# Kernel tuning notes

Hardware: AMD Instinct MI355X
Metric: run time of the kernel (lower is better)

The kernel has to match this reference:

```python
import jax, jax.numpy as jnp
import numpy as np

N, IN_DIM, H1, H2 = 12288, 512, 256, 128

def setup_inputs() -> dict:
    key = jax.random.key(0)
    k = jax.random.split(key, 6)
    glorot = lambda kk, fi, fo: jax.random.normal(kk, (fi, fo), jnp.float32) * np.sqrt(2.0 / (fi + fo))
    return {
        "X": jax.random.normal(k[0], (N, IN_DIM), jnp.float32),
        "adj": jax.random.uniform(k[1], (N, N), jnp.float32) / N,  # scaled like a normalized adjacency
        "noise": jax.random.normal(k[2], (N, H2), jnp.float32),
        "W0": glorot(k[3], IN_DIM, H1),
        "W_mu": glorot(k[4], H1, H2),
        "W_logstd": glorot(k[5], H1, H2),
    }

def reference(X, adj, noise, W0, W_mu, W_logstd):
    # GraphConvSparse layer 1: relu(adj @ (X @ W0))
    hidden = jax.nn.relu(adj @ (X @ W0))            # [N, H1]
    # mean / logstd heads (identity activation)
    mean = adj @ (hidden @ W_mu)                    # [N, H2]
    logstd = adj @ (hidden @ W_logstd)              # [N, H2]
    # reparameterization
    Z = noise * jnp.exp(logstd) + mean              # [N, H2]
    # dot-product decode
    A_pred = jax.nn.sigmoid(Z @ Z.T)                # [N, N]
    return A_pred
```

## Files before the change

kernel.cpp:

```cpp
#include <hip/hip_runtime.h>
#include <hip/hip_fp8.h>
#include <stdint.h>

#define NN 12288
#define IND 512
#define H1D 256
#define H2D 128

using bf16x8 = __attribute__((ext_vector_type(8))) short;
using f32x4  = __attribute__((ext_vector_type(4))) float;
using u32x4  = __attribute__((ext_vector_type(4))) unsigned int;

__device__ __forceinline__ unsigned short f2bf(float f){
  unsigned int u = __float_as_uint(f);
  return (unsigned short)((u + 0x7fffu + ((u >> 16) & 1u)) >> 16);
}
__device__ __forceinline__ float bf2f(unsigned short h){
  return __uint_as_float(((unsigned int)h) << 16);
}
__device__ __forceinline__ void gload_lds16(const void* g, void* l){
  __builtin_amdgcn_global_load_lds(
      (const __attribute__((address_space(1))) unsigned int*)(uintptr_t)g,
      (__attribute__((address_space(3))) unsigned int*)(unsigned int)(uintptr_t)l,
      16, 0, 0);
}
template<bool HI>
__device__ __forceinline__ unsigned cvt2(float a, float b, unsigned old){
#if __has_builtin(__builtin_amdgcn_cvt_pk_fp8_f32)
  return (unsigned)__builtin_amdgcn_cvt_pk_fp8_f32(a, b, (int)old, HI);
#else
  __hip_fp8_e4m3 pa(a), pb(b);
  unsigned v = (unsigned)pa.__x | ((unsigned)pb.__x << 8);
  return HI ? ((old & 0x0000FFFFu) | (v << 16)) : ((old & 0xFFFF0000u) | v);
#endif
}
__device__ __forceinline__ void sync0(){
  asm volatile("s_waitcnt vmcnt(0) lgkmcnt(0)" ::: "memory");
  __builtin_amdgcn_s_barrier();
  __builtin_amdgcn_sched_barrier(0);
}

__global__ __launch_bounds__(256) void k_cvt(const float* __restrict__ in,
                                             char* __restrict__ out,
                                             float scale, long n16){
  const long stride = (long)gridDim.x * 256;
  for (long i = (long)blockIdx.x * 256 + threadIdx.x; i < n16; i += stride){
    const f32x4* p = (const f32x4*)(in + i * 16);
    f32x4 a = __builtin_nontemporal_load(p);
    f32x4 b = __builtin_nontemporal_load(p + 1);
    f32x4 c = __builtin_nontemporal_load(p + 2);
    f32x4 d = __builtin_nontemporal_load(p + 3);
    u32x4 pk;
    pk[0] = cvt2<false>(a[0]*scale, a[1]*scale, 0u); pk[0] = cvt2<true>(a[2]*scale, a[3]*scale, pk[0]);
    pk[1] = cvt2<false>(b[0]*scale, b[1]*scale, 0u); pk[1] = cvt2<true>(b[2]*scale, b[3]*scale, pk[1]);
    pk[2] = cvt2<false>(c[0]*scale, c[1]*scale, 0u); pk[2] = cvt2<true>(c[2]*scale, c[3]*scale, pk[2]);
    pk[3] = cvt2<false>(d[0]*scale, d[1]*scale, 0u); pk[3] = cvt2<true>(d[2]*scale, d[3]*scale, pk[3]);
    *(u32x4*)(out + i * 16) = pk;
  }
}

__global__ __launch_bounds__(256) void k_w0t(const float* __restrict__ W0,
                                             char* __restrict__ W0T){
  __shared__ float Ls[64][65];
  const int t = (int)threadIdx.x;
  const int k0 = (int)blockIdx.x * 64;
  const int h0 = (int)blockIdx.y * 64;
  {
    const int r = t >> 2, c = (t & 3) * 16;
    const float* p = W0 + (size_t)(k0 + r) * H1D + h0 + c;
#pragma unroll
    for (int q = 0; q < 4; ++q)
      *(float4*)&Ls[r][c + q*4] = *(const float4*)(p + q*4);
  }
  __syncthreads();
  const int h = t >> 2, kc = (t & 3) * 16;
  u32x4 pk;
#pragma unroll
  for (int q = 0; q < 4; ++q){
    unsigned wv = cvt2<false>(Ls[kc+q*4+0][h], Ls[kc+q*4+1][h], 0u);
    wv = cvt2<true>(Ls[kc+q*4+2][h], Ls[kc+q*4+3][h], wv);
    pk[q] = wv;
  }
  *(u32x4*)(W0T + (size_t)(h0 + h) * IND + k0 + kc) = pk;
}

#define STAGE(BUF, SIDX) { \
  _Pragma("unroll") \
  for (int p = 0; p < 2; ++p) \
    gload_lds16(Ap + (size_t)(p*32) * lda + (size_t)(SIDX)*128, \
                Alds[BUF] + p*4096 + w*1024); \
  _Pragma("unroll") \
  for (int i = 0; i < 4; ++i) \
    gload_lds16(Bp + (size_t)(i*32) * ldb + (size_t)(SIDX)*128, \
                Blds[BUF] + i*4096 + w*1024); \
}

#define MF8(CUR) { \
  _Pragma("unroll") \
  for (int kk = 0; kk < 4; ++kk){ \
    long af[4]; long bfr[2]; \
    _Pragma("unroll") \
    for (int mi = 0; mi < 4; ++mi){ \
      int row = mi*16 + l15; \
      int off = row*128 + ((kk*32 + l16*8) ^ ((row & 7) << 4)); \
      af[mi] = *(const long*)(Alds[CUR] + off); \
    } \
    _Pragma("unroll") \
    for (int ni = 0; ni < 2; ++ni){ \
      int row = w*32 + ni*16 + l15; \
      int off = row*128 + ((kk*32 + l16*8) ^ ((row & 7) << 4)); \
      bfr[ni] = *(const long*)(Blds[CUR] + off); \
    } \
    _Pragma("unroll") \
    for (int mi = 0; mi < 4; ++mi) \
      _Pragma("unroll") \
      for (int ni = 0; ni < 2; ++ni) \
        acc[mi][ni] = __builtin_amdgcn_mfma_f32_16x16x32_fp8_fp8(af[mi], bfr[ni], acc[mi][ni], 0, 0, 0); \
  } }

template<int KSPLIT, int MODE>
__global__ __launch_bounds__(256, 3) void k_gf8(const char* __restrict__ A, int lda, int K,
                                                const char* __restrict__ Bt, int ldb,
                                                void* __restrict__ Out){
  __shared__ __align__(16) char Alds[2][64*128];
  __shared__ __align__(16) char Blds[2][128*128];
  const int t = (int)threadIdx.x;
  const int w = t >> 6, l = t & 63;
  const int l15 = l & 15, l16 = l >> 4;

  int khalf, idx;
  if (KSPLIT == 2){
    int f = (int)blockIdx.x, x = f & 7;
    khalf = x >> 2;
    idx = (f >> 3) * 4 + (x & 3);
  } else { khalf = 0; idx = (int)blockIdx.x; }
  const int m0 = (idx >> 1) * 64;
  const int nh = idx & 1;
  const size_t kb = (size_t)khalf * K;
  const int S = K >> 7;

  f32x4 acc[4][2];
#pragma unroll
  for (int mi = 0; mi < 4; ++mi)
#pragma unroll
    for (int ni = 0; ni < 2; ++ni) acc[mi][ni] = 0;

  const int swz = ((l & 7) ^ (l >> 3)) << 4;
  const char* Ap = A  + (size_t)(m0 + w*8 + (l >> 3)) * lda + kb + swz;
  const char* Bp = Bt + (size_t)(nh*128 + w*8 + (l >> 3)) * ldb + kb + swz;

  STAGE(0, 0);
  sync0();
  for (int s = 0; s < S; ++s){
    const int cur = s & 1;
    if (s + 1 < S){ if (cur == 0){ STAGE(1, s + 1); } else { STAGE(0, s + 1); } }
    if (cur == 0){ MF8(0); } else { MF8(1); }
    if (s + 1 < S) sync0();
  }

  if (MODE == 0){
    char* OutT = (char*)Out;
#pragma unroll
    for (int mi = 0; mi < 4; ++mi)
#pragma unroll
      for (int ni = 0; ni < 2; ++ni){
        int gr = m0 + mi*16 + l16*4;
        int gc = nh*128 + w*32 + ni*16 + l15;
        unsigned wd = cvt2<false>(acc[mi][ni][0], acc[mi][ni][1], 0u);
        wd = cvt2<true>(acc[mi][ni][2], acc[mi][ni][3], wd);
        *(unsigned*)(OutT + (size_t)gc * NN + gr) = wd;
      }
  } else {
    float* P = (float*)Out + (size_t)khalf * NN * H1D;
#pragma unroll
    for (int mi = 0; mi < 4; ++mi)
#pragma unroll
      for (int ni = 0; ni < 2; ++ni){
        int gr = m0 + mi*16 + l16*4;
        int gc = nh*128 + w*32 + ni*16 + l15;
#pragma unroll
        for (int v = 0; v < 4; ++v)
          P[(size_t)(gr + v) * H1D + gc] = acc[mi][ni][v];
      }
  }
}

__global__ __launch_bounds__(256) void k_combine_ht(const float* __restrict__ p0,
                                                    const float* __restrict__ p1,
                                                    char* __restrict__ HT){
  __shared__ float Ls[64][65];
  const int t = (int)threadIdx.x;
  const int n0 = (int)blockIdx.x * 64;
  const int h0 = (int)blockIdx.y * 64;
  const int lr = t >> 4, lc = (t & 15) * 4;
#pragma unroll
  for (int q = 0; q < 4; ++q){
    int n = lr + q*16;
    size_t idx = (size_t)(n0 + n) * H1D + h0 + lc;
    float4 a = *(const float4*)(p0 + idx);
    float4 b = *(const float4*)(p1 + idx);
    Ls[n][lc+0] = fmaxf(a.x + b.x, 0.f);
    Ls[n][lc+1] = fmaxf(a.y + b.y, 0.f);
    Ls[n][lc+2] = fmaxf(a.z + b.z, 0.f);
    Ls[n][lc+3] = fmaxf(a.w + b.w, 0.f);
  }
  __syncthreads();
  const int hr = t >> 2, nc = (t & 3) * 16;
  u32x4 pk;
#pragma unroll
  for (int q = 0; q < 4; ++q){
    unsigned wd = cvt2<false>(Ls[nc+q*4+0][hr], Ls[nc+q*4+1][hr], 0u);
    wd = cvt2<true>(Ls[nc+q*4+2][hr], Ls[nc+q*4+3][hr], wd);
    pk[q] = wd;
  }
  *(u32x4*)(HT + (size_t)(h0 + hr) * NN + n0 + nc) = pk;
}

__global__ __launch_bounds__(256) void k_heads(const float* __restrict__ p0,
                                               const float* __restrict__ Wmu,
                                               const float* __restrict__ Wls,
                                               const float* __restrict__ noise,
                                               unsigned short* __restrict__ Zhi,
                                               unsigned short* __restrict__ Zlo){
  __shared__ float AHs[32][256];
  __shared__ float Wms[32][128];
  __shared__ float Wlss[32][128];
  const float INV = 1.0f / 67108864.0f;
  const float* p1 = p0 + (size_t)NN * H1D;
  const int t  = (int)threadIdx.x;
  const int r0 = (int)blockIdx.x * 32;
  {
    const int r = t >> 3, c0 = (t & 7) * 32;
    size_t base = (size_t)(r0 + r) * H1D + c0;
#pragma unroll
    for (int q = 0; q < 8; ++q){
      float4 a = *(const float4*)(p0 + base + q*4);
      float4 b = *(const float4*)(p1 + base + q*4);
      AHs[r][c0 + q*4 + 0] = (a.x + b.x) * INV;
      AHs[r][c0 + q*4 + 1] = (a.y + b.y) * INV;
      AHs[r][c0 + q*4 + 2] = (a.z + b.z) * INV;
      AHs[r][c0 + q*4 + 3] = (a.w + b.w) * INV;
    }
  }
  const int j = t & 127, rg = t >> 7;
  float mu[16], ls[16];
#pragma unroll
  for (int r = 0; r < 16; ++r){ mu[r] = 0.f; ls[r] = 0.f; }

  for (int kc = 0; kc < 8; ++kc){
    __syncthreads();
    {
      const int r = t >> 3, c0 = (t & 7) * 16;
      const float* pm = Wmu + (size_t)(kc*32 + r) * H2D + c0;
      const float* pl = Wls + (size_t)(kc*32 + r) * H2D + c0;
#pragma unroll
      for (int q = 0; q < 4; ++q){
        *(float4*)&Wms[r][c0 + q*4]  = *(const float4*)(pm + q*4);
        *(float4*)&Wlss[r][c0 + q*4] = *(const float4*)(pl + q*4);
      }
    }
    __syncthreads();
#pragma unroll 4
    for (int k = 0; k < 32; ++k){
      float wm = Wms[k][j], wl = Wlss[k][j];
#pragma unroll
      for (int r = 0; r < 16; ++r){
        float a = AHs[rg*16 + r][kc*32 + k];
        mu[r] += a * wm;
        ls[r] += a * wl;
      }
    }
  }
#pragma unroll
  for (int r = 0; r < 16; ++r){
    const int i = r0 + rg*16 + r;
    float z = noise[(size_t)i * H2D + j] * __expf(ls[r]) + mu[r];
    unsigned short zh = f2bf(z);
    unsigned short zl = f2bf(z - bf2f(zh));
    Zhi[(size_t)i * H2D + j] = zh;
    Zlo[(size_t)i * H2D + j] = zl;
  }
}

__global__ __launch_bounds__(512) void k_decode(const unsigned short* __restrict__ Zhi,
                                                const unsigned short* __restrict__ Zlo,
                                                float* __restrict__ Out){
  __shared__ unsigned short T[4][128*64];
  const int t = (int)threadIdx.x;
  const int w = t >> 6, l = t & 63;
  const int l15 = l & 15, l16 = l >> 4;
  const int wr = w >> 2, wc = w & 3;
  const size_t m0 = (size_t)blockIdx.x * 128;
  const size_t n0 = (size_t)blockIdx.y * 128;

  f32x4 acc[4][2];
#pragma unroll
  for (int mi = 0; mi < 4; ++mi)
#pragma unroll
    for (int ni = 0; ni < 2; ++ni) acc[mi][ni] = 0;

#pragma unroll
  for (int p = 0; p < 2; ++p){
    if (p) __syncthreads();
#pragma unroll
    for (int i = 0; i < 2; ++i){
      int P = i*8192 + t*16;
      int row = P >> 7;
      int Li = (P & 127) ^ ((row & 7) << 4);
      size_t ga = (size_t)row * 256 + (size_t)p * 128 + Li;
      char* lb0 = (char*)T[0] + i*8192 + w*1024;
      char* lb1 = (char*)T[1] + i*8192 + w*1024;
      char* lb2 = (char*)T[2] + i*8192 + w*1024;
      char* lb3 = (char*)T[3] + i*8192 + w*1024;
      gload_lds16((const char*)Zhi + m0*256 + ga, lb0);
      gload_lds16((const char*)Zlo + m0*256 + ga, lb1);
      gload_lds16((const char*)Zhi + n0*256 + ga, lb2);
      gload_lds16((const char*)Zlo + n0*256 + ga, lb3);
    }
    __syncthreads();
#pragma unroll
    for (int kk = 0; kk < 2; ++kk){
      bf16x8 ah[4], al[4], bh[2], bl[2];
#pragma unroll
      for (int mi = 0; mi < 4; ++mi){
        int row = wr*64 + mi*16 + l15;
        int off = row*128 + ((kk*64 + l16*16) ^ ((row & 7) << 4));
        ah[mi] = *(const bf16x8*)((const char*)T[0] + off);
        al[mi] = *(const bf16x8*)((const char*)T[1] + off);
      }
#pragma unroll
      for (int ni = 0; ni < 2; ++ni){
        int row = wc*32 + ni*16 + l15;
        int off = row*128 + ((kk*64 + l16*16) ^ ((row & 7) << 4));
        bh[ni] = *(const bf16x8*)((const char*)T[2] + off);
        bl[ni] = *(const bf16x8*)((const char*)T[3] + off);
      }
#pragma unroll
      for (int mi = 0; mi < 4; ++mi)
#pragma unroll
        for (int ni = 0; ni < 2; ++ni){
          acc[mi][ni] = __builtin_amdgcn_mfma_f32_16x16x32_bf16(ah[mi], bh[ni], acc[mi][ni], 0, 0, 0);
          acc[mi][ni] = __builtin_amdgcn_mfma_f32_16x16x32_bf16(ah[mi], bl[ni], acc[mi][ni], 0, 0, 0);
          acc[mi][ni] = __builtin_amdgcn_mfma_f32_16x16x32_bf16(al[mi], bh[ni], acc[mi][ni], 0, 0, 0);
        }
    }
  }

#pragma unroll
  for (int mi = 0; mi < 4; ++mi)
#pragma unroll
    for (int ni = 0; ni < 2; ++ni){
      size_t gr = m0 + (size_t)(wr*64 + mi*16 + l16*4);
      size_t gc = n0 + (size_t)(wc*32 + ni*16 + l15);
#pragma unroll
      for (int v = 0; v < 4; ++v){
        float x = acc[mi][ni][v];
        float sg = 1.0f / (1.0f + __expf(-x));
        __builtin_nontemporal_store(sg, &Out[(gr + v) * (size_t)NN + gc]);
      }
    }
}

extern "C" void kernel_launch(void* const* d_in, const int* in_sizes, int n_in,
                              void* d_out, int out_size, void* d_ws, size_t ws_size,
                              hipStream_t stream) {
  const float* X     = (const float*)d_in[0];
  const float* adj   = (const float*)d_in[1];
  const float* noise = (const float*)d_in[2];
  const float* W0    = (const float*)d_in[3];
  const float* Wmu   = (const float*)d_in[4];
  const float* Wls   = (const float*)d_in[5];
  float* out = (float*)d_out;
  char* ws = (char*)d_ws;

  char*           XW0Tf8 = ws;
  char*           HidTf8 = ws + 3145728;
  char*           W0Tf8  = ws + 6291456;
  unsigned short* Zhi    = (unsigned short*)(ws + 6422528);
  unsigned short* Zlo    = (unsigned short*)(ws + 9568256);
  char*           Xf8    = ws + 12713984;
  char*  adjf8 = (char*)d_out;
  float* part  = (float*)((char*)d_out + 150994944);

  const float S_ADJ = 8192.0f;

  k_cvt<<<2048, 256, 0, stream>>>(adj, adjf8, S_ADJ, (long)NN * NN / 16);
  k_w0t<<<dim3(8, 4), 256, 0, stream>>>(W0, W0Tf8);
  k_cvt<<<256, 256, 0, stream>>>(X, Xf8, 1.0f, (long)NN * IND / 16);
  k_gf8<1,0><<<384, 256, 0, stream>>>(Xf8, IND, IND, W0Tf8, IND, (void*)XW0Tf8);
  k_gf8<2,1><<<768, 256, 0, stream>>>(adjf8, NN, 6144, XW0Tf8, NN, (void*)part);
  k_combine_ht<<<dim3(192, 4), 256, 0, stream>>>(part, part + (size_t)NN * H1D, HidTf8);
  k_gf8<2,1><<<768, 256, 0, stream>>>(adjf8, NN, 6144, HidTf8, NN, (void*)part);
  k_heads<<<384, 256, 0, stream>>>(part, Wmu, Wls, noise, Zhi, Zlo);
  k_decode<<<dim3(96, 96), 512, 0, stream>>>(Zhi, Zlo, out);
}
```

Baseline: 616.6 us.

## Triple-buffer LDS in FP8 GEMM to prefetch two K-stages ahead

Moves the fp8 GEMM main loop from double-buffered to triple-buffered LDS staging. Global-to-LDS loads are issued two K-steps ahead, and a partial vmcnt wait (6 outstanding loads) lets the next stage's loads stay in flight across the barrier. The aim is to hide more global-memory latency behind the MFMA work. In exchange, LDS use rises from 48KB to 72KB per block and launch bounds drop from 3 to 2 blocks per CU, which lowers occupancy.

```diff
diff --git a/kernel.cpp b/kernel.cpp
--- a/kernel.cpp
+++ b/kernel.cpp
@@ -33,11 +33,6 @@
   unsigned v = (unsigned)pa.__x | ((unsigned)pb.__x << 8);
   return HI ? ((old & 0x0000FFFFu) | (v << 16)) : ((old & 0xFFFF0000u) | v);
 #endif
-}
-__device__ __forceinline__ void sync0(){
-  asm volatile("s_waitcnt vmcnt(0) lgkmcnt(0)" ::: "memory");
-  __builtin_amdgcn_s_barrier();
-  __builtin_amdgcn_sched_barrier(0);
 }
 
 __global__ __launch_bounds__(256) void k_cvt(const float* __restrict__ in,
@@ -85,17 +80,19 @@
 }
 
 #define STAGE(BUF, SIDX) { \
+  char* Ad = Alds[BUF] + w*1024; \
+  char* Bd = Blds[BUF] + w*1024; \
   _Pragma("unroll") \
   for (int p = 0; p < 2; ++p) \
-    gload_lds16(Ap + (size_t)(p*32) * lda + (size_t)(SIDX)*128, \
-                Alds[BUF] + p*4096 + w*1024); \
+    gload_lds16(Ap + (size_t)(p*32) * lda + (size_t)(SIDX)*128, Ad + p*4096); \
   _Pragma("unroll") \
   for (int i = 0; i < 4; ++i) \
-    gload_lds16(Bp + (size_t)(i*32) * ldb + (size_t)(SIDX)*128, \
-                Blds[BUF] + i*4096 + w*1024); \
+    gload_lds16(Bp + (size_t)(i*32) * ldb + (size_t)(SIDX)*128, Bd + i*4096); \
 }
 
 #define MF8(CUR) { \
+  const char* Ab = Alds[CUR]; \
+  const char* Bb = Blds[CUR]; \
   _Pragma("unroll") \
   for (int kk = 0; kk < 4; ++kk){ \
     long af[4]; long bfr[2]; \
@@ -103,13 +100,13 @@
     for (int mi = 0; mi < 4; ++mi){ \
       int row = mi*16 + l15; \
       int off = row*128 + ((kk*32 + l16*8) ^ ((row & 7) << 4)); \
-      af[mi] = *(const long*)(Alds[CUR] + off); \
+      af[mi] = *(const long*)(Ab + off); \
     } \
     _Pragma("unroll") \
     for (int ni = 0; ni < 2; ++ni){ \
       int row = w*32 + ni*16 + l15; \
       int off = row*128 + ((kk*32 + l16*8) ^ ((row & 7) << 4)); \
-      bfr[ni] = *(const long*)(Blds[CUR] + off); \
+      bfr[ni] = *(const long*)(Bb + off); \
     } \
     _Pragma("unroll") \
     for (int mi = 0; mi < 4; ++mi) \
@@ -119,11 +116,11 @@
   } }
 
 template<int KSPLIT, int MODE>
-__global__ __launch_bounds__(256, 3) void k_gf8(const char* __restrict__ A, int lda, int K,
+__global__ __launch_bounds__(256, 2) void k_gf8(const char* __restrict__ A, int lda, int K,
                                                 const char* __restrict__ Bt, int ldb,
                                                 void* __restrict__ Out){
-  __shared__ __align__(16) char Alds[2][64*128];
-  __shared__ __align__(16) char Blds[2][128*128];
+  __shared__ __align__(16) char Alds[3][64*128];
+  __shared__ __align__(16) char Blds[3][128*128];
   const int t = (int)threadIdx.x;
   const int w = t >> 6, l = t & 63;
   const int l15 = l & 15, l16 = l >> 4;
@@ -150,12 +147,28 @@
   const char* Bp = Bt + (size_t)(nh*128 + w*8 + (l >> 3)) * ldb + kb + swz;
 
   STAGE(0, 0);
-  sync0();
+  if (S > 1){
+    STAGE(1, 1);
+    asm volatile("s_waitcnt vmcnt(6) lgkmcnt(0)" ::: "memory");
+  } else {
+    asm volatile("s_waitcnt vmcnt(0) lgkmcnt(0)" ::: "memory");
+  }
+  __builtin_amdgcn_s_barrier();
+  __builtin_amdgcn_sched_barrier(0);
+
+  int cur = 0;
   for (int s = 0; s < S; ++s){
-    const int cur = s & 1;
-    if (s + 1 < S){ if (cur == 0){ STAGE(1, s + 1); } else { STAGE(0, s + 1); } }
-    if (cur == 0){ MF8(0); } else { MF8(1); }
-    if (s + 1 < S) sync0();
+    const bool have2 = (s + 2 < S);
+    int nxt2 = cur + 2; if (nxt2 >= 3) nxt2 -= 3;
+    if (have2) STAGE(nxt2, s + 2);
+    MF8(cur);
+    if (s + 1 < S){
+      if (have2) asm volatile("s_waitcnt vmcnt(6) lgkmcnt(0)" ::: "memory");
+      else       asm volatile("s_waitcnt vmcnt(0) lgkmcnt(0)" ::: "memory");
+      __builtin_amdgcn_s_barrier();
+      __builtin_amdgcn_sched_barrier(0);
+    }
+    ++cur; if (cur >= 3) cur -= 3;
   }
 
   if (MODE == 0){
```

New measurement: 636.0 us. 1.03x slower.

## Exploit symmetry of Z·Zᵀ in decode, compute upper triangle and mirror tiles

Applied to the files above, without the earlier changes.

The decode kernel now computes only the tiles with by >= bx. Each off-diagonal tile is transposed through LDS after its direct store and written to the mirrored location, which roughly halves the MFMA work and the Z tile loads. Because half the blocks exit immediately, load balance suffers somewhat. The extra LDS transpose and the second pass of strided stores also add work, and the output write volume stays the same.

```diff
diff --git a/kernel.cpp b/kernel.cpp
--- a/kernel.cpp
+++ b/kernel.cpp
@@ -285,13 +285,18 @@
 __global__ __launch_bounds__(512) void k_decode(const unsigned short* __restrict__ Zhi,
                                                 const unsigned short* __restrict__ Zlo,
                                                 float* __restrict__ Out){
-  __shared__ unsigned short T[4][128*64];
+  const int bx = (int)blockIdx.x, by = (int)blockIdx.y;
+  if (by < bx) return;
+  __shared__ __align__(16) char SMEM[65536];
+  unsigned short* T0 = (unsigned short*)SMEM;
+  float (*Ls)[133] = (float(*)[133])SMEM;
+
   const int t = (int)threadIdx.x;
   const int w = t >> 6, l = t & 63;
   const int l15 = l & 15, l16 = l >> 4;
   const int wr = w >> 2, wc = w & 3;
-  const size_t m0 = (size_t)blockIdx.x * 128;
-  const size_t n0 = (size_t)blockIdx.y * 128;
+  const size_t m0 = (size_t)bx * 128;
+  const size_t n0 = (size_t)by * 128;
 
   f32x4 acc[4][2];
 #pragma unroll
@@ -308,14 +313,11 @@
       int row = P >> 7;
       int Li = (P & 127) ^ ((row & 7) << 4);
       size_t ga = (size_t)row * 256 + (size_t)p * 128 + Li;
-      char* lb0 = (char*)T[0] + i*8192 + w*1024;
-      char* lb1 = (char*)T[1] + i*8192 + w*1024;
-      char* lb2 = (char*)T[2] + i*8192 + w*1024;
-      char* lb3 = (char*)T[3] + i*8192 + w*1024;
-      gload_lds16((const char*)Zhi + m0*256 + ga, lb0);
-      gload_lds16((const char*)Zlo + m0*256 + ga, lb1);
-      gload_lds16((const char*)Zhi + n0*256 + ga, lb2);
-      gload_lds16((const char*)Zlo + n0*256 + ga, lb3);
+      char* lb = (char*)T0 + i*8192 + w*1024;
+      gload_lds16((const char*)Zhi + m0*256 + ga, lb);
+      gload_lds16((const char*)Zlo + m0*256 + ga, lb + 16384);
+      gload_lds16((const char*)Zhi + n0*256 + ga, lb + 32768);
+      gload_lds16((const char*)Zlo + n0*256 + ga, lb + 49152);
     }
     __syncthreads();
 #pragma unroll
@@ -325,15 +327,15 @@
       for (int mi = 0; mi < 4; ++mi){
         int row = wr*64 + mi*16 + l15;
         int off = row*128 + ((kk*64 + l16*16) ^ ((row & 7) << 4));
-        ah[mi] = *(const bf16x8*)((const char*)T[0] + off);
-        al[mi] = *(const bf16x8*)((const char*)T[1] + off);
+        ah[mi] = *(const bf16x8*)((const char*)T0 + off);
+        al[mi] = *(const bf16x8*)((const char*)T0 + 16384 + off);
       }
 #pragma unroll
       for (int ni = 0; ni < 2; ++ni){
         int row = wc*32 + ni*16 + l15;
         int off = row*128 + ((kk*64 + l16*16) ^ ((row & 7) << 4));
-        bh[ni] = *(const bf16x8*)((const char*)T[2] + off);
-        bl[ni] = *(const bf16x8*)((const char*)T[3] + off);
+        bh[ni] = *(const bf16x8*)((const char*)T0 + 32768 + off);
+        bl[ni] = *(const bf16x8*)((const char*)T0 + 49152 + off);
       }
 #pragma unroll
       for (int mi = 0; mi < 4; ++mi)
@@ -354,11 +356,39 @@
       size_t gc = n0 + (size_t)(wc*32 + ni*16 + l15);
 #pragma unroll
       for (int v = 0; v < 4; ++v){
-        float x = acc[mi][ni][v];
-        float sg = 1.0f / (1.0f + __expf(-x));
+        float sg = 1.0f / (1.0f + __expf(-acc[mi][ni][v]));
+        acc[mi][ni][v] = sg;
         __builtin_nontemporal_store(sg, &Out[(gr + v) * (size_t)NN + gc]);
       }
     }
+
+  if (by == bx) return;
+
+#pragma unroll
+  for (int p = 0; p < 2; ++p){
+    __syncthreads();
+    if (wr == p){
+#pragma unroll
+      for (int mi = 0; mi < 4; ++mi)
+#pragma unroll
+        for (int ni = 0; ni < 2; ++ni)
+#pragma unroll
+          for (int v = 0; v < 4; ++v)
+            Ls[mi*16 + l16*4 + v][wc*32 + ni*16 + l15] = acc[mi][ni][v];
+    }
+    __syncthreads();
+    const int a = t >> 2;
+    const int b0 = (t & 3) * 16;
+    float vv[16];
+#pragma unroll
+    for (int k = 0; k < 16; ++k) vv[k] = Ls[b0 + k][a];
+    float* dst = &Out[(n0 + a) * (size_t)NN + m0 + (size_t)(p*64 + b0)];
+#pragma unroll
+    for (int q = 0; q < 4; ++q){
+      f32x4 pk = { vv[q*4+0], vv[q*4+1], vv[q*4+2], vv[q*4+3] };
+      __builtin_nontemporal_store(pk, (f32x4*)(dst + q*4));
+    }
+  }
 }
 
 extern "C" void kernel_launch(void* const* d_in, const int* in_sizes, int n_in,
```

Measured after the change: 921.8 us. 1.49x slower.
